# Kernel tuning notes

Hardware: AMD Instinct MI355X
Metric: run time of the kernel (lower is better)

## Reference

```python
import jax, jax.numpy as jnp
import numpy as np
import math

B, N, T, F_IN, F_OUT = 8, 512, 12, 32, 64


def setup_inputs() -> dict:
    key = jax.random.key(0)
    k1, k2, k3, k4, k5 = jax.random.split(key, 5)
    x = jax.random.normal(k1, (B, N, T, F_IN), dtype=jnp.float32)
    phaseAct_matrix = jax.random.uniform(k2, (B, T, N, N), dtype=jnp.float32)
    adj = jax.random.uniform(k3, (N, N), dtype=jnp.float32)  # sym-normalized adjacency stand-in
    mask = (jax.random.uniform(k4, (N,)) < 0.5).astype(jnp.float32)  # 1 = observed node, 0 = unknown
    theta = jax.random.normal(k5, (F_IN, F_OUT), dtype=jnp.float32) * 0.05
    return {"x": x, "phaseAct_matrix": phaseAct_matrix, "adj": adj, "mask": mask, "theta": theta}


def _spatial_attention(x):
    # x: (B, N, T, F) -> scores (B, T, N, N)
    f = x.shape[-1]
    xt = x.transpose(0, 2, 1, 3)  # (B, T, N, F)
    score = jnp.einsum('btnf,btmf->btnm', xt, xt) / math.sqrt(f)
    return jax.nn.softmax(score, axis=-1)


def reference(x, phaseAct_matrix, adj, mask, theta):
    f = x.shape[-1]
    t_steps = x.shape[2]
    inv_sqrt_f = 1.0 / math.sqrt(f)
    m = mask[None, :, None, None]  # broadcast over (B, N, T-1, F)

    def body(i, x_cur):
        sa = _spatial_attention(x_cur) * inv_sqrt_f          # (B, T, N, N)
        sat_act = (phaseAct_matrix * sa).transpose(0, 1, 3, 2)  # (B, T, N, N) transposed
        xt = x_cur.transpose(0, 2, 1, 3)                     # (B, T, N, F)
        # predict step t from step t-1: (B, T-1, N, F)
        x_pred = jnp.einsum('btnm,btmf->btnf', sat_act[:, 1:], xt[:, :t_steps - 1])
        x_pred = x_pred.transpose(0, 2, 1, 3)                # (B, N, T-1, F)
        # revise_unknown: keep observed nodes, impute unknown nodes at steps 1..T-1
        x_rev = x_cur[:, :, 1:, :] * m + x_pred * (1.0 - m)
        return jnp.concatenate([x_cur[:, :, 0:1, :], x_rev], axis=2)

    x = jax.lax.fori_loop(1, t_steps, body, x)

    sa = _spatial_attention(x) * inv_sqrt_f                  # (B, T, N, N)
    satAct_adj = phaseAct_matrix * adj[None, None] * sa      # (B, T, N, N)
    xt = x.transpose(0, 2, 1, 3)                             # (B, T, N, F)
    agg = jnp.einsum('btmn,btmf->btnf', satAct_adj, xt)      # transpose(adj) @ x
    out = jax.nn.relu(jnp.einsum('btnf,fo->btno', agg, theta))  # (B, T, N, F_out)
    return out.transpose(0, 2, 1, 3)                         # (B, N, T, F_out)
```

## Files before the change

### kernel.cpp

```cpp
#include <hip/hip_runtime.h>


#define B_ 8
#define N_ 512
#define T_ 12
#define F_ 32
#define O_ 64
#define MT 8

typedef unsigned int uint_t;
typedef unsigned short ushort_t;
typedef _Float16 f16_t;
typedef _Float16 f16x4 __attribute__((ext_vector_type(4)));
typedef _Float16 f16x8 __attribute__((ext_vector_type(8)));
typedef float f32x4 __attribute__((ext_vector_type(4)));

__device__ __forceinline__ void atomAddF(float* p, float v) {
    __hip_atomic_fetch_add(p, v, __ATOMIC_RELAXED, __HIP_MEMORY_SCOPE_AGENT);
}

#define LGKM_BARRIER() asm volatile("s_waitcnt lgkmcnt(0)\n\ts_barrier" ::: "memory")

__device__ __forceinline__ int xidx(int b, int n, int t, int f) {
    return ((b * N_ + n) * T_ + t) * F_ + f;
}
__device__ __forceinline__ f16x8 load_frag8(const float* p) {
    float4 a = *reinterpret_cast<const float4*>(p);
    float4 b = *reinterpret_cast<const float4*>(p + 4);
    f16x8 r;
    r[0] = (f16_t)a.x; r[1] = (f16_t)a.y; r[2] = (f16_t)a.z; r[3] = (f16_t)a.w;
    r[4] = (f16_t)b.x; r[5] = (f16_t)b.y; r[6] = (f16_t)b.z; r[7] = (f16_t)b.w;
    return r;
}
union U2H4 { uint2 u; f16x4 h; };

__global__ __launch_bounds__(256)
void permute_kernel(const float* __restrict__ src, ushort_t* __restrict__ dst)
{
    __shared__ float Lp[16][516];
    const int tid = threadIdx.x;
    const int mc  = blockIdx.x;
    const int s   = blockIdx.y;
    src += (size_t)s * N_ * N_ + (size_t)mc * 16 * N_;
    uint_t* dstu = (uint_t*)dst + (size_t)s * 131072 + (size_t)mc * 4096;

    #pragma unroll
    for (int k = 0; k < 32; ++k) {
        int idx = tid + 256 * k;
        Lp[idx >> 9][idx & 511] = src[idx];
    }
    __syncthreads();
    #pragma unroll
    for (int k = 0; k < 16; ++k) {
        int u    = tid + 256 * k;
        int nt   = u >> 7;
        int r    = u & 127;
        int quad = r >> 5;
        int cl   = (r >> 1) & 15;
        int m0   = quad * 4 + (r & 1) * 2;
        int n    = nt * 16 + cl;
        union { f16_t h[2]; uint_t i; } pk;
        pk.h[0] = (f16_t)Lp[m0][n];
        pk.h[1] = (f16_t)Lp[m0 + 1][n];
        dstu[u] = pk.i;
    }
}

template <int FINAL>
__global__ __launch_bounds__(512)
void gcn_kernel(const float* __restrict__ x0,
                const float* __restrict__ xcur,
                float* __restrict__ dst,
                const ushort_t* __restrict__ phase_h,
                const ushort_t* __restrict__ adj_h,
                const float* __restrict__ mask)
{
    __shared__ float st[4][16];

    const int tid  = threadIdx.x;
    const int w    = tid >> 6;
    const int l    = tid & 63;
    const int quad = l >> 4;
    const int col  = l & 15;
    const int mt   = blockIdx.x;
    const int t    = FINAL ? blockIdx.y : blockIdx.y + 1;
    const int b    = blockIdx.z;
    const int nt0  = w * 4;
    const float inv_f = 0.17677669529663687f;

    const float* xs = (FINAL && t == 0) ? x0 : xcur;
    const float* xp = FINAL ? xs : ((t == 1) ? x0 : xcur);
    const int    tp = FINAL ? t : t - 1;

    if (tid < 64) ((float*)st)[tid] = 0.f;

    f16x8 bf[4];
    #pragma unroll
    for (int i = 0; i < 4; ++i)
        bf[i] = load_frag8(&xs[xidx(b, (nt0 + i) * 16 + col, t, quad * 8)]);

    const uint_t* phu = (const uint_t*)phase_h + (size_t)(b * T_ + t) * 131072;
    const uint_t* adu = (const uint_t*)adj_h;

    f16x8 af = load_frag8(&xs[xidx(b, mt * 64 + col, t, quad * 8)]);
    f16x4 bp[2];
    #pragma unroll
    for (int fh = 0; fh < 2; ++fh)
        #pragma unroll
        for (int j = 0; j < 4; ++j)
            bp[fh][j] = (f16_t)xp[xidx(b, mt * 64 + quad * 4 + j, tp, fh * 16 + col)];
    uint2 ph[4], aj[4];
    #pragma unroll
    for (int i = 0; i < 4; ++i) {
        ph[i] = *(const uint2*)(phu + (size_t)(mt * 4) * 4096 + (nt0 + i) * 128 + l * 2);
        if (FINAL)
            aj[i] = *(const uint2*)(adu + (size_t)(mt * 4) * 4096 + (nt0 + i) * 128 + l * 2);
    }

    f32x4 acc[4][2];
    #pragma unroll
    for (int i = 0; i < 4; ++i) {
        acc[i][0] = (f32x4){0.f, 0.f, 0.f, 0.f};
        acc[i][1] = (f32x4){0.f, 0.f, 0.f, 0.f};
    }

    LGKM_BARRIER();

    for (int c = 0; c < 4; ++c) {
        f32x4 s4[4];
        #pragma unroll
        for (int i = 0; i < 4; ++i)
            s4[i] = __builtin_amdgcn_mfma_f32_16x16x32_f16(
                        af, bf[i], (f32x4){0.f, 0.f, 0.f, 0.f}, 0, 0, 0);

        const int c2  = (c < 3) ? c + 1 : c;
        const int mb2 = mt * 64 + c2 * 16;
        f16x8 af_n = load_frag8(&xs[xidx(b, mb2 + col, t, quad * 8)]);
        f16x4 bp_n[2];
        #pragma unroll
        for (int fh = 0; fh < 2; ++fh)
            #pragma unroll
            for (int j = 0; j < 4; ++j)
                bp_n[fh][j] = (f16_t)xp[xidx(b, mb2 + quad * 4 + j, tp, fh * 16 + col)];
        uint2 ph_n[4], aj_n[4];
        #pragma unroll
        for (int i = 0; i < 4; ++i) {
            ph_n[i] = *(const uint2*)(phu + (size_t)(mt * 4 + c2) * 4096 + (nt0 + i) * 128 + l * 2);
            if (FINAL)
                aj_n[i] = *(const uint2*)(adu + (size_t)(mt * 4 + c2) * 4096 + (nt0 + i) * 128 + l * 2);
        }

        float e[4][4], sw[4];
        #pragma unroll
        for (int v = 0; v < 4; ++v) {
            #pragma unroll
            for (int i = 0; i < 4; ++i)
                e[i][v] = __expf(fminf(s4[i][v] * inv_f, 60.f));
            sw[v] = (e[0][v] + e[1][v]) + (e[2][v] + e[3][v]);
        }
        #pragma unroll
        for (int d = 1; d < 16; d <<= 1)
            #pragma unroll
            for (int v = 0; v < 4; ++v)
                sw[v] += __shfl_xor(sw[v], d, 64);
        if (col < 4) {
            float sv = (col == 0) ? sw[0] : (col == 1) ? sw[1] : (col == 2) ? sw[2] : sw[3];
            atomicAdd(&st[c][quad * 4 + col], sv);
        }

        #pragma unroll
        for (int i = 0; i < 4; ++i) {
            U2H4 P; P.u = ph[i];
            if (FINAL) {
                U2H4 A; A.u = aj[i];
                #pragma unroll
                for (int v = 0; v < 4; ++v) e[i][v] *= (float)P.h[v] * (float)A.h[v];
            } else {
                #pragma unroll
                for (int v = 0; v < 4; ++v) e[i][v] *= (float)P.h[v];
            }
        }

        LGKM_BARRIER();

        f32x4 rs = *(const f32x4*)&st[c][quad * 4];
        f32x4 bet;
        #pragma unroll
        for (int v = 0; v < 4; ++v) bet[v] = inv_f * __builtin_amdgcn_rcpf(rs[v]);
        #pragma unroll
        for (int i = 0; i < 4; ++i) {
            f16x4 wf;
            #pragma unroll
            for (int v = 0; v < 4; ++v) wf[v] = (f16_t)(e[i][v] * bet[v]);
            #pragma unroll
            for (int fh = 0; fh < 2; ++fh)
                acc[i][fh] = __builtin_amdgcn_mfma_f32_16x16x16f16(wf, bp[fh], acc[i][fh], 0, 0, 0);
        }

        af = af_n;
        bp[0] = bp_n[0]; bp[1] = bp_n[1];
        #pragma unroll
        for (int i = 0; i < 4; ++i) { ph[i] = ph_n[i]; if (FINAL) aj[i] = aj_n[i]; }
    }

    #pragma unroll
    for (int i = 0; i < 4; ++i) {
        #pragma unroll
        for (int v = 0; v < 4; ++v) {
            const int n = (nt0 + i) * 16 + quad * 4 + v;
            if (FINAL) {
                float* d0 = &dst[((b * T_ + t) * N_ + n) * F_ + col];
                atomAddF(d0,      acc[i][0][v]);
                atomAddF(d0 + 16, acc[i][1][v]);
            } else if (mask[n] == 0.f) {
                atomAddF(&dst[xidx(b, n, t, col)],      acc[i][0][v]);
                atomAddF(&dst[xidx(b, n, t, 16 + col)], acc[i][1][v]);
            }
        }
    }
    if (!FINAL && mt == 0) {
        for (int p = tid; p < N_ * F_; p += 512) {
            int n = p >> 5, f = p & 31;
            if (mask[n] != 0.f) dst[xidx(b, n, t, f)] = xcur[xidx(b, n, t, f)];
        }
    }
}

__global__ __launch_bounds__(256)
void proj_kernel(const float* __restrict__ agg, const float* __restrict__ theta,
                 float* __restrict__ out)
{
    __shared__ float th[F_ * O_];
    int tid = threadIdx.x;
    #pragma unroll
    for (int p = 0; p < 8; ++p) th[tid + 256 * p] = theta[tid + 256 * p];
    __syncthreads();
    int g  = blockIdx.x * 256 + tid;
    int o  = g & 63;
    int r  = g >> 6;
    int tt = r % T_;
    int r2 = r / T_;
    int n  = r2 & 511;
    int b  = r2 >> 9;
    const float* a = &agg[((b * T_ + tt) * N_ + n) * F_];
    float s = 0.f;
    #pragma unroll
    for (int f = 0; f < F_; ++f) s += a[f] * th[f * O_ + o];
    out[g] = fmaxf(s, 0.f);
}

extern "C" void kernel_launch(void* const* d_in, const int* in_sizes, int n_in,
                              void* d_out, int out_size, void* d_ws, size_t ws_size,
                              hipStream_t stream)
{
    const float* x     = (const float*)d_in[0];
    const float* phase = (const float*)d_in[1];
    const float* adj   = (const float*)d_in[2];
    const float* mask  = (const float*)d_in[3];
    const float* theta = (const float*)d_in[4];
    float* out = (float*)d_out;

    const size_t XE = (size_t)B_ * N_ * T_ * F_;
    float*    bufs    = (float*)d_ws;
    float*    agg     = bufs + (size_t)11 * XE;
    ushort_t* phase_h = (ushort_t*)(bufs + (size_t)12 * XE);
    ushort_t* adj_h   = phase_h + (size_t)96 * N_ * N_;

    hipMemsetAsync(bufs, 0, (size_t)12 * XE * sizeof(float), stream);
    permute_kernel<<<dim3(32, 96), 256, 0, stream>>>(phase, phase_h);
    permute_kernel<<<dim3(32, 1), 256, 0, stream>>>(adj, adj_h);

    const float* cur = x;
    for (int i = 0; i < T_ - 1; ++i) {
        float* nxt = bufs + (size_t)i * XE;
        gcn_kernel<0><<<dim3(MT, T_ - 1, B_), 512, 0, stream>>>(
            x, cur, nxt, phase_h, adj_h, mask);
        cur = nxt;
    }
    gcn_kernel<1><<<dim3(MT, T_, B_), 512, 0, stream>>>(
        x, cur, agg, phase_h, adj_h, mask);
    proj_kernel<<<(B_ * N_ * T_ * O_) / 256, 256, 0, stream>>>(agg, theta, out);
}
```

Measured before the change: 1.091 ms.

## Split softmax into row-sum pass and atomic-free prediction pass over all sources

Each fused step kernel is replaced by two kernels. A rowsum kernel computes the softmax denominators for every source row into a buffer. A prediction kernel then gives each wave one destination tile, loops over all source tiles, and writes results directly. This removes the global float atomics, the large workspace memset and the in-block LDS reduction and barriers. In exchange the attention scores are computed twice, and each step now costs two launches plus a longer serial loop per wave with less parallelism per block.

```diff
diff --git a/kernel.cpp b/kernel.cpp
--- a/kernel.cpp
+++ b/kernel.cpp
@@ -6,7 +6,6 @@
 #define T_ 12
 #define F_ 32
 #define O_ 64
-#define MT 8
 
 typedef unsigned int uint_t;
 typedef unsigned short ushort_t;
@@ -14,12 +13,6 @@
 typedef _Float16 f16x4 __attribute__((ext_vector_type(4)));
 typedef _Float16 f16x8 __attribute__((ext_vector_type(8)));
 typedef float f32x4 __attribute__((ext_vector_type(4)));
-
-__device__ __forceinline__ void atomAddF(float* p, float v) {
-    __hip_atomic_fetch_add(p, v, __ATOMIC_RELAXED, __HIP_MEMORY_SCOPE_AGENT);
-}
-
-#define LGKM_BARRIER() asm volatile("s_waitcnt lgkmcnt(0)\n\ts_barrier" ::: "memory")
 
 __device__ __forceinline__ int xidx(int b, int n, int t, int f) {
     return ((b * N_ + n) * T_ + t) * F_ + f;
@@ -67,161 +60,150 @@
 }
 
 template <int FINAL>
-__global__ __launch_bounds__(512)
-void gcn_kernel(const float* __restrict__ x0,
-                const float* __restrict__ xcur,
-                float* __restrict__ dst,
-                const ushort_t* __restrict__ phase_h,
-                const ushort_t* __restrict__ adj_h,
-                const float* __restrict__ mask)
-{
-    __shared__ float st[4][16];
-
+__global__ __launch_bounds__(256)
+void rowsum_kernel(const float* __restrict__ x0,
+                   const float* __restrict__ xcur,
+                   float* __restrict__ rsinv)
+{
     const int tid  = threadIdx.x;
     const int w    = tid >> 6;
     const int l    = tid & 63;
     const int quad = l >> 4;
     const int col  = l & 15;
-    const int mt   = blockIdx.x;
     const int t    = FINAL ? blockIdx.y : blockIdx.y + 1;
     const int b    = blockIdx.z;
-    const int nt0  = w * 4;
+    const int mtile = blockIdx.x * 4 + w;
+    const float inv_f = 0.17677669529663687f;
+
+    const float* xs = (FINAL && t == 0) ? x0 : xcur;
+
+    f16x8 af = load_frag8(&xs[xidx(b, mtile * 16 + col, t, quad * 8)]);
+    f16x8 bf = load_frag8(&xs[xidx(b, col, t, quad * 8)]);
+
+    float sw[4] = {0.f, 0.f, 0.f, 0.f};
+    for (int nt = 0; nt < 32; ++nt) {
+        const int nt2 = (nt < 31) ? nt + 1 : nt;
+        f16x8 bf_n = load_frag8(&xs[xidx(b, nt2 * 16 + col, t, quad * 8)]);
+        f32x4 s4 = __builtin_amdgcn_mfma_f32_16x16x32_f16(
+                       af, bf, (f32x4){0.f, 0.f, 0.f, 0.f}, 0, 0, 0);
+        #pragma unroll
+        for (int v = 0; v < 4; ++v)
+            sw[v] += __expf(fminf(s4[v] * inv_f, 60.f));
+        bf = bf_n;
+    }
+    #pragma unroll
+    for (int d = 1; d < 16; d <<= 1)
+        #pragma unroll
+        for (int v = 0; v < 4; ++v)
+            sw[v] += __shfl_xor(sw[v], d, 64);
+    if (col < 4) {
+        float sv = (col == 0) ? sw[0] : (col == 1) ? sw[1] : (col == 2) ? sw[2] : sw[3];
+        rsinv[((size_t)(b * T_ + t)) * N_ + mtile * 16 + quad * 4 + col] =
+            inv_f * __builtin_amdgcn_rcpf(sv);
+    }
+}
+
+template <int FINAL>
+__global__ __launch_bounds__(256)
+void pred_kernel(const float* __restrict__ x0,
+                 const float* __restrict__ xcur,
+                 float* __restrict__ dst,
+                 const ushort_t* __restrict__ phase_h,
+                 const ushort_t* __restrict__ adj_h,
+                 const float* __restrict__ rsinv,
+                 const float* __restrict__ mask)
+{
+    const int tid  = threadIdx.x;
+    const int w    = tid >> 6;
+    const int l    = tid & 63;
+    const int quad = l >> 4;
+    const int col  = l & 15;
+    const int t    = FINAL ? blockIdx.y : blockIdx.y + 1;
+    const int b    = blockIdx.z;
+    const int ntg  = blockIdx.x * 4 + w;
+    const int n0   = ntg * 16;
     const float inv_f = 0.17677669529663687f;
 
     const float* xs = (FINAL && t == 0) ? x0 : xcur;
     const float* xp = FINAL ? xs : ((t == 1) ? x0 : xcur);
     const int    tp = FINAL ? t : t - 1;
 
-    if (tid < 64) ((float*)st)[tid] = 0.f;
-
-    f16x8 bf[4];
-    #pragma unroll
-    for (int i = 0; i < 4; ++i)
-        bf[i] = load_frag8(&xs[xidx(b, (nt0 + i) * 16 + col, t, quad * 8)]);
-
-    const uint_t* phu = (const uint_t*)phase_h + (size_t)(b * T_ + t) * 131072;
-    const uint_t* adu = (const uint_t*)adj_h;
-
-    f16x8 af = load_frag8(&xs[xidx(b, mt * 64 + col, t, quad * 8)]);
+    f16x8 bf = load_frag8(&xs[xidx(b, n0 + col, t, quad * 8)]);
+
+    const uint_t* php = (const uint_t*)phase_h + (size_t)(b * T_ + t) * 131072
+                        + ntg * 128 + l * 2;
+    const uint_t* adp = (const uint_t*)adj_h + ntg * 128 + l * 2;
+    const float*  rsv = rsinv + (size_t)(b * T_ + t) * N_;
+
+    f16x8 af = load_frag8(&xs[xidx(b, col, t, quad * 8)]);
     f16x4 bp[2];
     #pragma unroll
     for (int fh = 0; fh < 2; ++fh)
         #pragma unroll
         for (int j = 0; j < 4; ++j)
-            bp[fh][j] = (f16_t)xp[xidx(b, mt * 64 + quad * 4 + j, tp, fh * 16 + col)];
-    uint2 ph[4], aj[4];
-    #pragma unroll
-    for (int i = 0; i < 4; ++i) {
-        ph[i] = *(const uint2*)(phu + (size_t)(mt * 4) * 4096 + (nt0 + i) * 128 + l * 2);
-        if (FINAL)
-            aj[i] = *(const uint2*)(adu + (size_t)(mt * 4) * 4096 + (nt0 + i) * 128 + l * 2);
-    }
-
-    f32x4 acc[4][2];
-    #pragma unroll
-    for (int i = 0; i < 4; ++i) {
-        acc[i][0] = (f32x4){0.f, 0.f, 0.f, 0.f};
-        acc[i][1] = (f32x4){0.f, 0.f, 0.f, 0.f};
-    }
-
-    LGKM_BARRIER();
-
-    for (int c = 0; c < 4; ++c) {
-        f32x4 s4[4];
-        #pragma unroll
-        for (int i = 0; i < 4; ++i)
-            s4[i] = __builtin_amdgcn_mfma_f32_16x16x32_f16(
-                        af, bf[i], (f32x4){0.f, 0.f, 0.f, 0.f}, 0, 0, 0);
-
-        const int c2  = (c < 3) ? c + 1 : c;
-        const int mb2 = mt * 64 + c2 * 16;
-        f16x8 af_n = load_frag8(&xs[xidx(b, mb2 + col, t, quad * 8)]);
+            bp[fh][j] = (f16_t)xp[xidx(b, quad * 4 + j, tp, fh * 16 + col)];
+    uint2 ph = *(const uint2*)php;
+    uint2 aj;
+    if (FINAL) aj = *(const uint2*)adp;
+    f32x4 rs4 = *(const f32x4*)(rsv + quad * 4);
+
+    f32x4 acc0 = (f32x4){0.f, 0.f, 0.f, 0.f};
+    f32x4 acc1 = (f32x4){0.f, 0.f, 0.f, 0.f};
+
+    for (int mc = 0; mc < 32; ++mc) {
+        f32x4 s4 = __builtin_amdgcn_mfma_f32_16x16x32_f16(
+                       af, bf, (f32x4){0.f, 0.f, 0.f, 0.f}, 0, 0, 0);
+
+        const int mc2 = (mc < 31) ? mc + 1 : mc;
+        f16x8 af_n = load_frag8(&xs[xidx(b, mc2 * 16 + col, t, quad * 8)]);
         f16x4 bp_n[2];
         #pragma unroll
         for (int fh = 0; fh < 2; ++fh)
             #pragma unroll
             for (int j = 0; j < 4; ++j)
-                bp_n[fh][j] = (f16_t)xp[xidx(b, mb2 + quad * 4 + j, tp, fh * 16 + col)];
-        uint2 ph_n[4], aj_n[4];
-        #pragma unroll
-        for (int i = 0; i < 4; ++i) {
-            ph_n[i] = *(const uint2*)(phu + (size_t)(mt * 4 + c2) * 4096 + (nt0 + i) * 128 + l * 2);
-            if (FINAL)
-                aj_n[i] = *(const uint2*)(adu + (size_t)(mt * 4 + c2) * 4096 + (nt0 + i) * 128 + l * 2);
-        }
-
-        float e[4][4], sw[4];
-        #pragma unroll
-        for (int v = 0; v < 4; ++v) {
-            #pragma unroll
-            for (int i = 0; i < 4; ++i)
-                e[i][v] = __expf(fminf(s4[i][v] * inv_f, 60.f));
-            sw[v] = (e[0][v] + e[1][v]) + (e[2][v] + e[3][v]);
-        }
-        #pragma unroll
-        for (int d = 1; d < 16; d <<= 1)
+                bp_n[fh][j] = (f16_t)xp[xidx(b, mc2 * 16 + quad * 4 + j, tp, fh * 16 + col)];
+        uint2 ph_n = *(const uint2*)(php + (size_t)mc2 * 4096);
+        uint2 aj_n;
+        if (FINAL) aj_n = *(const uint2*)(adp + (size_t)mc2 * 4096);
+        f32x4 rs4_n = *(const f32x4*)(rsv + mc2 * 16 + quad * 4);
+
+        U2H4 P; P.u = ph;
+        f16x4 wf;
+        if (FINAL) {
+            U2H4 A; A.u = aj;
             #pragma unroll
             for (int v = 0; v < 4; ++v)
-                sw[v] += __shfl_xor(sw[v], d, 64);
-        if (col < 4) {
-            float sv = (col == 0) ? sw[0] : (col == 1) ? sw[1] : (col == 2) ? sw[2] : sw[3];
-            atomicAdd(&st[c][quad * 4 + col], sv);
+                wf[v] = (f16_t)(__expf(fminf(s4[v] * inv_f, 60.f)) * rs4[v]
+                                * (float)P.h[v] * (float)A.h[v]);
+        } else {
+            #pragma unroll
+            for (int v = 0; v < 4; ++v)
+                wf[v] = (f16_t)(__expf(fminf(s4[v] * inv_f, 60.f)) * rs4[v]
+                                * (float)P.h[v]);
         }
-
-        #pragma unroll
-        for (int i = 0; i < 4; ++i) {
-            U2H4 P; P.u = ph[i];
-            if (FINAL) {
-                U2H4 A; A.u = aj[i];
-                #pragma unroll
-                for (int v = 0; v < 4; ++v) e[i][v] *= (float)P.h[v] * (float)A.h[v];
-            } else {
-                #pragma unroll
-                for (int v = 0; v < 4; ++v) e[i][v] *= (float)P.h[v];
+        acc0 = __builtin_amdgcn_mfma_f32_16x16x16f16(wf, bp[0], acc0, 0, 0, 0);
+        acc1 = __builtin_amdgcn_mfma_f32_16x16x16f16(wf, bp[1], acc1, 0, 0, 0);
+
+        af = af_n; bp[0] = bp_n[0]; bp[1] = bp_n[1];
+        ph = ph_n; rs4 = rs4_n;
+        if (FINAL) aj = aj_n;
+    }
+
+    #pragma unroll
+    for (int v = 0; v < 4; ++v) {
+        const int n = n0 + quad * 4 + v;
+        float p0 = acc0[v], p1 = acc1[v];
+        if (FINAL) {
+            float* d0 = &dst[((size_t)(b * T_ + t) * N_ + n) * F_ + col];
+            d0[0]  = p0;
+            d0[16] = p1;
+        } else {
+            if (mask[n] != 0.f) {
+                p0 = xcur[xidx(b, n, t, col)];
+                p1 = xcur[xidx(b, n, t, col + 16)];
             }
-        }
-
-        LGKM_BARRIER();
-
-        f32x4 rs = *(const f32x4*)&st[c][quad * 4];
-        f32x4 bet;
-        #pragma unroll
-        for (int v = 0; v < 4; ++v) bet[v] = inv_f * __builtin_amdgcn_rcpf(rs[v]);
-        #pragma unroll
-        for (int i = 0; i < 4; ++i) {
-            f16x4 wf;
-            #pragma unroll
-            for (int v = 0; v < 4; ++v) wf[v] = (f16_t)(e[i][v] * bet[v]);
-            #pragma unroll
-            for (int fh = 0; fh < 2; ++fh)
-                acc[i][fh] = __builtin_amdgcn_mfma_f32_16x16x16f16(wf, bp[fh], acc[i][fh], 0, 0, 0);
-        }
-
-        af = af_n;
-        bp[0] = bp_n[0]; bp[1] = bp_n[1];
-        #pragma unroll
-        for (int i = 0; i < 4; ++i) { ph[i] = ph_n[i]; if (FINAL) aj[i] = aj_n[i]; }
-    }
-
-    #pragma unroll
-    for (int i = 0; i < 4; ++i) {
-        #pragma unroll
-        for (int v = 0; v < 4; ++v) {
-            const int n = (nt0 + i) * 16 + quad * 4 + v;
-            if (FINAL) {
-                float* d0 = &dst[((b * T_ + t) * N_ + n) * F_ + col];
-                atomAddF(d0,      acc[i][0][v]);
-                atomAddF(d0 + 16, acc[i][1][v]);
-            } else if (mask[n] == 0.f) {
-                atomAddF(&dst[xidx(b, n, t, col)],      acc[i][0][v]);
-                atomAddF(&dst[xidx(b, n, t, 16 + col)], acc[i][1][v]);
-            }
-        }
-    }
-    if (!FINAL && mt == 0) {
-        for (int p = tid; p < N_ * F_; p += 512) {
-            int n = p >> 5, f = p & 31;
-            if (mask[n] != 0.f) dst[xidx(b, n, t, f)] = xcur[xidx(b, n, t, f)];
+            dst[xidx(b, n, t, col)]      = p0;
+            dst[xidx(b, n, t, col + 16)] = p1;
         }
     }
 }
@@ -265,19 +247,21 @@
     float*    agg     = bufs + (size_t)11 * XE;
     ushort_t* phase_h = (ushort_t*)(bufs + (size_t)12 * XE);
     ushort_t* adj_h   = phase_h + (size_t)96 * N_ * N_;
-
-    hipMemsetAsync(bufs, 0, (size_t)12 * XE * sizeof(float), stream);
+    float*    rs      = (float*)(adj_h + (size_t)N_ * N_);
+
     permute_kernel<<<dim3(32, 96), 256, 0, stream>>>(phase, phase_h);
     permute_kernel<<<dim3(32, 1), 256, 0, stream>>>(adj, adj_h);
 
     const float* cur = x;
     for (int i = 0; i < T_ - 1; ++i) {
         float* nxt = bufs + (size_t)i * XE;
-        gcn_kernel<0><<<dim3(MT, T_ - 1, B_), 512, 0, stream>>>(
-            x, cur, nxt, phase_h, adj_h, mask);
+        rowsum_kernel<0><<<dim3(8, T_ - 1, B_), 256, 0, stream>>>(x, cur, rs);
+        pred_kernel<0><<<dim3(8, T_ - 1, B_), 256, 0, stream>>>(
+            x, cur, nxt, phase_h, adj_h, rs, mask);
         cur = nxt;
     }
-    gcn_kernel<1><<<dim3(MT, T_, B_), 512, 0, stream>>>(
-        x, cur, agg, phase_h, adj_h, mask);
+    rowsum_kernel<1><<<dim3(8, T_, B_), 256, 0, stream>>>(x, cur, rs);
+    pred_kernel<1><<<dim3(8, T_, B_), 256, 0, stream>>>(
+        x, cur, agg, phase_h, adj_h, rs, mask);
     proj_kernel<<<(B_ * N_ * T_ * O_) / 256, 256, 0, stream>>>(agg, theta, out);
 }
```

Measured after the change: 1.079 ms. About the same (-1.1%).
